# Kernel tuning notes

Hardware: AMD Instinct MI355X
Metric: run time of the kernel (lower is better)

## Reference

```python
import jax, jax.numpy as jnp
import numpy as np

N, H, W, M = 1, 128, 128, 16
HID, STY, CIN, NC, COL = 256, 256, 128, 7, 64


def _lrelu(v):
    return jnp.where(v > 0, v, 0.2 * v)


def _conv(x, w, b=None):
    y = jax.lax.conv_general_dilated(x, w, (1, 1), 'SAME',
                                     dimension_numbers=('NCHW', 'OIHW', 'NCHW'))
    return y if b is None else y + b[None, :, None, None]


def _modlin(f, z, Wt, Wa, ba, Wb, bb):
    # ModLinear, bias=False, mod_bias=True, output_mode=True:
    # y = (f * alpha) @ W^T + beta
    alpha = z @ Wa.T + ba          # [N, in]
    beta = z @ Wb.T + bb           # [N, out]
    return jnp.einsum('nsi,oi->nso', f * alpha[:, None, :], Wt) + beta[:, None, :]


def setup_inputs() -> dict:
    key = jax.random.key(0)
    k = jax.random.split(key, 24)
    s = lambda f: np.float32(1.0 / np.sqrt(f))
    inp = {}
    inp['x'] = jax.random.normal(k[0], (N, H, W, M, CIN), jnp.float32)
    inp['m'] = jax.random.uniform(k[1], (N, H, W, M, NC), jnp.float32)
    inp['z'] = jax.random.normal(k[2], (N, STY), jnp.float32)
    inp['dists'] = jax.random.uniform(k[3], (N, H, W, M), jnp.float32) * 0.05
    # RenderMLP params
    inp['w1'] = jax.random.normal(k[4], (HID, CIN)) * s(CIN)
    inp['b1'] = jnp.zeros((HID,), jnp.float32)
    inp['wma'] = jax.random.normal(k[5], (HID, NC)) * s(NC)
    # 5 stacked ModLinears (fc_2, fc_3, fc_4, fc_5, fc_6)
    inp['ml_w'] = jax.random.normal(k[6], (5, HID, HID)) * s(HID)
    inp['ml_wa'] = jax.random.normal(k[7], (5, HID, STY)) * s(STY)
    inp['ml_ba'] = jnp.ones((5, HID), jnp.float32)
    inp['ml_wb'] = jax.random.normal(k[8], (5, HID, STY)) * s(STY)
    inp['ml_bb'] = jnp.zeros((5, HID), jnp.float32)
    inp['wsig'] = jax.random.normal(k[9], (1, HID)) * s(HID)
    inp['bsig'] = jnp.zeros((1,), jnp.float32)
    inp['wc'] = jax.random.normal(k[10], (COL, HID)) * s(HID)
    inp['bc'] = jnp.zeros((COL,), jnp.float32)
    # RenderCNN params
    inp['wz'] = jax.random.normal(k[11], (4 * HID, STY)) * s(STY)
    inp['bz'] = jnp.zeros((4 * HID,), jnp.float32)
    inp['c1_w'] = jax.random.normal(k[12], (HID, COL, 1, 1)) * s(COL)
    inp['c1_b'] = jnp.zeros((HID,), jnp.float32)
    inp['c2a_w'] = jax.random.normal(k[13], (HID, HID, 3, 3)) * s(HID * 9)
    inp['c2a_b'] = jnp.zeros((HID,), jnp.float32)
    inp['c2b_w'] = jax.random.normal(k[14], (HID, HID, 3, 3)) * s(HID * 9)
    inp['c3a_w'] = jax.random.normal(k[15], (HID, HID, 3, 3)) * s(HID * 9)
    inp['c3a_b'] = jnp.zeros((HID,), jnp.float32)
    inp['c3b_w'] = jax.random.normal(k[16], (HID, HID, 3, 3)) * s(HID * 9)
    inp['c4a_w'] = jax.random.normal(k[17], (HID, HID, 1, 1)) * s(HID)
    inp['c4a_b'] = jnp.zeros((HID,), jnp.float32)
    inp['c4b_w'] = jax.random.normal(k[18], (HID, HID, 1, 1)) * s(HID)
    inp['c4b_b'] = jnp.zeros((HID,), jnp.float32)
    inp['c4_w'] = jax.random.normal(k[19], (3, HID, 1, 1)) * s(HID)
    inp['c4_b'] = jnp.zeros((3,), jnp.float32)
    return inp


def reference(x, m, z, dists, w1, b1, wma, ml_w, ml_wa, ml_ba, ml_wb, ml_bb,
              wsig, bsig, wc, bc, wz, bz, c1_w, c1_b, c2a_w, c2a_b, c2b_w,
              c3a_w, c3a_b, c3b_w, c4a_w, c4a_b, c4b_w, c4b_b, c4_w, c4_b):
    n, h, w_, mm, cin = x.shape
    xf = x.reshape(n, -1, cin)              # [N, S, 128], S = H*W*M
    mf = m.reshape(n, -1, m.shape[-1])      # [N, S, 7]
    # RenderMLP
    f = jnp.einsum('nsi,oi->nso', xf, w1) + b1 + jnp.einsum('nsi,oi->nso', mf, wma)
    f = _lrelu(f)
    for i in range(3):  # fc_2, fc_3, fc_4
        f = _lrelu(_modlin(f, z, ml_w[i], ml_wa[i], ml_ba[i], ml_wb[i], ml_bb[i]))
    sigma = jnp.einsum('nsi,oi->nso', f, wsig) + bsig   # [N, S, 1]
    for i in (3, 4):    # fc_5, fc_6
        f = _lrelu(_modlin(f, z, ml_w[i], ml_wa[i], ml_ba[i], ml_wb[i], ml_bb[i]))
    c = jnp.einsum('nsi,oi->nso', f, wc) + bc           # [N, S, 64]
    # Volumetric alpha compositing along the M ray samples
    sigma = sigma.reshape(n, h, w_, mm)
    c = c.reshape(n, h, w_, mm, -1)
    alpha = 1.0 - jnp.exp(-jax.nn.relu(sigma) * dists)  # [N,H,W,M]
    t = jnp.cumprod(1.0 - alpha + 1e-10, axis=-1)
    t_excl = jnp.concatenate([jnp.ones_like(t[..., :1]), t[..., :-1]], axis=-1)
    wgt = alpha * t_excl
    feat = jnp.einsum('nhwm,nhwmc->nchw', wgt, c)       # [N, 64, H, W]
    # RenderCNN with style modulation
    zc = z @ wz.T + bz
    a0, a1, a2, a3 = jnp.split(zc, 4, axis=-1)
    mod = lambda y, wm, bm: y * (wm[:, :, None, None] + 1.0) + bm[:, :, None, None]
    y = _lrelu(_conv(feat, c1_w, c1_b))
    y = y + _conv(_lrelu(_conv(y, c2a_w, c2a_b)), c2b_w)
    y = _lrelu(mod(y, a0, a1))
    y = y + _conv(_lrelu(_conv(y, c3a_w, c3a_b)), c3b_w)
    y = _lrelu(mod(y, a2, a3))
    y = y + _conv(_lrelu(_conv(y, c4a_w, c4a_b)), c4b_w, c4b_b)
    y = _lrelu(y)
    return _conv(y, c4_w, c4_b)  # [N, 3, H, W]
```

## Files before the change

kernel.cpp:

```cpp
#include <hip/hip_runtime.h>
#include <hip/hip_bf16.h>

#define NPIX 16384
#define S_TOT 262144

typedef __attribute__((ext_vector_type(8))) short bf16x8;
typedef __attribute__((ext_vector_type(4))) float f32x4;

__device__ __forceinline__ float lrelu(float v) { return fmaxf(v, 0.2f * v); }
__device__ __forceinline__ unsigned short f2b(float f) {
  unsigned u = __float_as_uint(f);
  return (unsigned short)((u + 0x7FFFu + ((u >> 16) & 1u)) >> 16);
}
__device__ __forceinline__ unsigned cvtpk(float a, float b) {
  return (unsigned)f2b(a) | ((unsigned)f2b(b) << 16);
}
__device__ __forceinline__ float b2f(short s) {
  return __uint_as_float(((unsigned)(unsigned short)s) << 16);
}
__device__ __forceinline__ float f_lo(int u) { return __uint_as_float((unsigned)u << 16); }
__device__ __forceinline__ float f_hi(int u) { return __uint_as_float((unsigned)u & 0xffff0000u); }

__device__ float g_alpha[5 * 256];
__device__ float g_biasall[1600];
__device__ float g_amod[1024];
__device__ float g_sigma[S_TOT];
__device__ short g_c[S_TOT * 64];
__device__ short g_featb[NPIX * 64];
__device__ short g_y1[NPIX * 256];
__device__ short g_y2[NPIX * 256];
__device__ short g_y3[NPIX * 256];
__device__ short g_t [NPIX * 256];
__device__ short g_wpack[389120];
#define O_C1  0
#define O_C2A 16384
#define O_C2B (16384 + 589824)
#define O_C3A (16384 + 2 * 589824)
#define O_C3B (16384 + 3 * 589824)
#define O_C4A (16384 + 4 * 589824)
#define O_C4B (16384 + 4 * 589824 + 65536)
__device__ short g_wpack2[2506752];

__global__ __launch_bounds__(256) void kparams(const float* __restrict__ z,
    const float* __restrict__ wa, const float* __restrict__ ba,
    const float* __restrict__ wb, const float* __restrict__ bb,
    const float* __restrict__ wz, const float* __restrict__ bz,
    const float* __restrict__ b1, const float* __restrict__ bc) {
  __shared__ float zs[256];
  const int t = threadIdx.x;
  zs[t] = z[t];
  __syncthreads();
  g_biasall[t] = b1[t];
  if (t < 64) g_biasall[1536 + t] = bc[t];
  for (int l = 0; l < 5; ++l) {
    float accA = ba[l * 256 + t];
    float accB = bb[l * 256 + t];
    const float* rowA = wa + (l * 256 + t) * 256;
    const float* rowB = wb + (l * 256 + t) * 256;
    for (int k = 0; k < 256; k += 4) {
      float4 va = *(const float4*)(rowA + k);
      float4 vb = *(const float4*)(rowB + k);
      accA += va.x * zs[k] + va.y * zs[k + 1] + va.z * zs[k + 2] + va.w * zs[k + 3];
      accB += vb.x * zs[k] + vb.y * zs[k + 1] + vb.z * zs[k + 2] + vb.w * zs[k + 3];
    }
    g_alpha[l * 256 + t] = accA;
    g_biasall[256 + l * 256 + t] = accB;
  }
  for (int j = t; j < 1024; j += 256) {
    float acc = bz[j];
    const float* row = wz + j * 256;
    for (int k = 0; k < 256; k += 4) {
      float4 v = *(const float4*)(row + k);
      acc += v.x * zs[k] + v.y * zs[k + 1] + v.z * zs[k + 2] + v.w * zs[k + 3];
    }
    g_amod[j] = acc;
  }
}

__global__ __launch_bounds__(256) void kprep(
    const float* __restrict__ w1, const float* __restrict__ wma,
    const float* __restrict__ mlw, const float* __restrict__ wc,
    const float* __restrict__ wsig) {
  const int idx = blockIdx.x * 256 + threadIdx.x;
  float val;
  if (idx < 40960) {
    int mt = idx / 2560, r2 = idx % 2560;
    int ks = r2 / 512, r = r2 % 512;
    int ln = r >> 3, j = r & 7;
    int oc = mt * 16 + (ln & 15);
    int k = ks * 32 + (ln >> 4) * 8 + j;
    val = (k < 128) ? w1[oc * 128 + k] : ((k < 135) ? wma[oc * 7 + (k - 128)] : 0.f);
  } else if (idx < 368640) {
    int t = idx - 40960;
    int l = t / 65536, t2 = t % 65536;
    int mt = t2 / 4096, r2 = t2 % 4096;
    int ks = r2 / 512, r = r2 % 512;
    int ln = r >> 3, j = r & 7;
    int oc = mt * 16 + (ln & 15);
    int k = ks * 32 + (ln >> 4) * 8 + j;
    val = mlw[l * 65536 + oc * 256 + k] * g_alpha[l * 256 + k];
  } else if (idx < 385024) {
    int t = idx - 368640;
    int mt = t / 4096, r2 = t % 4096;
    int ks = r2 / 512, r = r2 % 512;
    int ln = r >> 3, j = r & 7;
    int oc = mt * 16 + (ln & 15);
    int k = ks * 32 + (ln >> 4) * 8 + j;
    val = wc[oc * 256 + k];
  } else {
    int t = idx - 385024;
    int ks = t / 512, r = t % 512;
    int ln = r >> 3, j = r & 7;
    int row = ln & 15;
    int k = ks * 32 + (ln >> 4) * 8 + j;
    val = (row == 0) ? wsig[k] : 0.f;
  }
  g_wpack[idx] = (short)f2b(val);
}

__global__ __launch_bounds__(256) void kprep_cnn(
    const float* __restrict__ c1w,
    const float* __restrict__ c2aw, const float* __restrict__ c2bw,
    const float* __restrict__ c3aw, const float* __restrict__ c3bw,
    const float* __restrict__ c4aw, const float* __restrict__ c4bw) {
  const int idx = blockIdx.x * 256 + threadIdx.x;
  float val;
  if (idx < 16384) {
    int mt = idx / 1024, r2 = idx % 1024;
    int ks = r2 / 512, r = r2 % 512;
    int ln = r >> 3, j = r & 7;
    int oc = mt * 16 + (ln & 15);
    int k = ks * 32 + (ln >> 4) * 8 + j;
    val = c1w[oc * 64 + k];
  } else if (idx < O_C4A) {
    int t = idx - 16384;
    int cv = t / 589824, t2 = t % 589824;
    const float* w = (cv == 0) ? c2aw : (cv == 1) ? c2bw : (cv == 2) ? c3aw : c3bw;
    int mt = t2 / 36864, r2 = t2 % 36864;
    int ks = r2 / 512, r = r2 % 512;
    int ln = r >> 3, j = r & 7;
    int oc = mt * 16 + (ln & 15);
    int k = ks * 32 + (ln >> 4) * 8 + j;
    int tap = k >> 8, ic = k & 255;
    val = w[oc * 2304 + ic * 9 + tap];
  } else {
    int t = idx - O_C4A;
    const float* w = (t < 65536) ? c4aw : c4bw;
    int t2 = t & 65535;
    int mt = t2 / 4096, r2 = t2 % 4096;
    int ks = r2 / 512, r = r2 % 512;
    int ln = r >> 3, j = r & 7;
    int oc = mt * 16 + (ln & 15);
    int k = ks * 32 + (ln >> 4) * 8 + j;
    val = w[oc * 256 + k];
  }
  g_wpack2[idx] = (short)f2b(val);
}

__device__ __forceinline__ bf16x8 ldsB(const short* buf, int s, int kbyte) {
  const char* p = (const char*)buf + s * 512 + (kbyte ^ ((s & 7) << 4));
  return *(const bf16x8*)p;
}
__device__ __forceinline__ bf16x8 ldA(const short* gA, int frag, int lane) {
  return *(const bf16x8*)(gA + ((size_t)frag << 9) + lane * 8);
}

template<int KS>
__device__ __forceinline__ void layer_gemm(const short* __restrict__ gA,
    const short* __restrict__ inb, short* __restrict__ outb,
    const float* __restrict__ bias, int lane, int wm, int wn) {
  const int lrow = lane & 15;
  const int lkb = (lane >> 4) * 16;
  const int rb = (lane >> 4) * 4;
  f32x4 acc[4][4];
#pragma unroll
  for (int mi = 0; mi < 4; ++mi) {
    const f32x4 bv = *(const f32x4*)(bias + (wm * 4 + mi) * 16 + rb);
#pragma unroll
    for (int ni = 0; ni < 4; ++ni) acc[mi][ni] = bv;
  }
#pragma unroll
  for (int ks = 0; ks < KS; ++ks) {
    bf16x8 A[4], B[4];
#pragma unroll
    for (int mi = 0; mi < 4; ++mi)
      A[mi] = ldA(gA, (wm * 4 + mi) * KS + ks, lane);
#pragma unroll
    for (int ni = 0; ni < 4; ++ni)
      B[ni] = ldsB(inb, wn * 64 + ni * 16 + lrow, ks * 64 + lkb);
#pragma unroll
    for (int mi = 0; mi < 4; ++mi)
#pragma unroll
      for (int ni = 0; ni < 4; ++ni)
        acc[mi][ni] = __builtin_amdgcn_mfma_f32_16x16x32_bf16(A[mi], B[ni], acc[mi][ni], 0, 0, 0);
  }
#pragma unroll
  for (int mi = 0; mi < 4; ++mi) {
    const int oc0 = (wm * 4 + mi) * 16 + rb;
#pragma unroll
    for (int ni = 0; ni < 4; ++ni) {
      const int s = wn * 64 + ni * 16 + lrow;
      f32x4 a = acc[mi][ni];
      char* p = (char*)outb + s * 512 + ((oc0 * 2) ^ ((s & 7) << 4));
      *(int2*)p = make_int2((int)cvtpk(lrelu(a[0]), lrelu(a[1])),
                            (int)cvtpk(lrelu(a[2]), lrelu(a[3])));
    }
  }
}

__global__ __launch_bounds__(512, 1) void kmlp_mfma(
    const float* __restrict__ x, const float* __restrict__ m_in,
    const float* __restrict__ bsig) {
  __shared__ short fbuf[2][32768];
  __shared__ float bias_all[1600];
  const int tid = threadIdx.x;
  const int lane = tid & 63, w = tid >> 6;
  const int wm = w & 3, wn = w >> 2;
  const int s0 = blockIdx.x * 128;

  {
    const float* xp = x + (size_t)s0 * 128;
    const int s = tid >> 2, c = tid & 3;
#pragma unroll
    for (int e = 0; e < 4; ++e) {
      float4 f0 = *(const float4*)(xp + s * 128 + c * 32 + e * 8);
      float4 f1 = *(const float4*)(xp + s * 128 + c * 32 + e * 8 + 4);
      int4 pk;
      pk.x = (int)cvtpk(f0.x, f0.y); pk.y = (int)cvtpk(f0.z, f0.w);
      pk.z = (int)cvtpk(f1.x, f1.y); pk.w = (int)cvtpk(f1.z, f1.w);
      char* p = (char*)fbuf[0] + s * 512 + ((c * 64 + e * 16) ^ ((s & 7) << 4));
      *(int4*)p = pk;
    }
  }
  if (tid < 128) {
    const float* mp = m_in + (size_t)(s0 + tid) * 7;
    float mv[8];
#pragma unroll
    for (int q = 0; q < 7; ++q) mv[q] = mp[q];
    mv[7] = 0.f;
    int4 pk;
    pk.x = (int)cvtpk(mv[0], mv[1]); pk.y = (int)cvtpk(mv[2], mv[3]);
    pk.z = (int)cvtpk(mv[4], mv[5]); pk.w = (int)cvtpk(mv[6], mv[7]);
    char* base = (char*)fbuf[0] + tid * 512;
    const int swz = (tid & 7) << 4;
    *(int4*)(base + (256 ^ swz)) = pk;
    int4 zz = make_int4(0, 0, 0, 0);
    *(int4*)(base + (272 ^ swz)) = zz;
    *(int4*)(base + (288 ^ swz)) = zz;
    *(int4*)(base + (304 ^ swz)) = zz;
  }
  for (int i = tid; i < 1600; i += 512) bias_all[i] = g_biasall[i];
  __syncthreads();

  layer_gemm<5>(g_wpack,                     fbuf[0], fbuf[1], bias_all,        lane, wm, wn);
  __syncthreads();
  layer_gemm<8>(g_wpack + 40960,             fbuf[1], fbuf[0], bias_all + 256,  lane, wm, wn);
  __syncthreads();
  layer_gemm<8>(g_wpack + 40960 + 65536,     fbuf[0], fbuf[1], bias_all + 512,  lane, wm, wn);
  __syncthreads();
  layer_gemm<8>(g_wpack + 40960 + 2 * 65536, fbuf[1], fbuf[0], bias_all + 768,  lane, wm, wn);
  __syncthreads();
  {
    const short* gS = g_wpack + 385024;
    const int lrow = lane & 15, lkb = (lane >> 4) * 16;
    f32x4 sacc = {0.f, 0.f, 0.f, 0.f};
#pragma unroll
    for (int ks = 0; ks < 8; ++ks) {
      bf16x8 A = ldA(gS, ks, lane);
      bf16x8 B = ldsB(fbuf[0], w * 16 + lrow, ks * 64 + lkb);
      sacc = __builtin_amdgcn_mfma_f32_16x16x32_bf16(A, B, sacc, 0, 0, 0);
    }
    if (lane < 16) g_sigma[s0 + w * 16 + lane] = sacc[0] + bsig[0];
  }
  layer_gemm<8>(g_wpack + 40960 + 3 * 65536, fbuf[0], fbuf[1], bias_all + 1024, lane, wm, wn);
  __syncthreads();
  layer_gemm<8>(g_wpack + 40960 + 4 * 65536, fbuf[1], fbuf[0], bias_all + 1280, lane, wm, wn);
  __syncthreads();
  {
    const int lrow = lane & 15, lkb = (lane >> 4) * 16;
    const int rb = (lane >> 4) * 4;
    const int oc0 = wm * 16 + rb;
    const f32x4 bv = *(const f32x4*)(bias_all + 1536 + oc0);
    f32x4 acc[4] = {bv, bv, bv, bv};
    const short* gA = g_wpack + 368640;
#pragma unroll
    for (int ks = 0; ks < 8; ++ks) {
      bf16x8 A = ldA(gA, wm * 8 + ks, lane);
#pragma unroll
      for (int ni = 0; ni < 4; ++ni) {
        bf16x8 B = ldsB(fbuf[0], wn * 64 + ni * 16 + lrow, ks * 64 + lkb);
        acc[ni] = __builtin_amdgcn_mfma_f32_16x16x32_bf16(A, B, acc[ni], 0, 0, 0);
      }
    }
#pragma unroll
    for (int ni = 0; ni < 4; ++ni) {
      const int s = wn * 64 + ni * 16 + lrow;
      *(int2*)(g_c + (size_t)(s0 + s) * 64 + oc0) =
          make_int2((int)cvtpk(acc[ni][0], acc[ni][1]),
                    (int)cvtpk(acc[ni][2], acc[ni][3]));
    }
  }
}

__global__ __launch_bounds__(256) void kcomposite(const float* __restrict__ dists) {
  const int tid = threadIdx.x;
  const int p = blockIdx.x * 4 + (tid >> 6);
  const int ch = tid & 63;
  const int base = p * 16;
  float T = 1.f, acc = 0.f;
  for (int mm = 0; mm < 16; ++mm) {
    float sgm = g_sigma[base + mm];
    float d = dists[base + mm];
    float a = 1.f - expf(-fmaxf(sgm, 0.f) * d);
    acc += a * T * b2f(g_c[(size_t)(base + mm) * 64 + ch]);
    T *= (1.f - a + 1e-10f);
  }
  g_featb[p * 64 + ch] = (short)f2b(acc);
}

template<int IC>
__global__ __launch_bounds__(256, 2) void kgemm1x1(const short* __restrict__ in,
    const short* __restrict__ gA, const float* __restrict__ bias,
    short* __restrict__ out) {
  constexpr int KS = IC / 32;
  constexpr int ROWB = IC * 2;
  __shared__ short binb[32 * IC];
  const int tid = threadIdx.x;
  const int lane = tid & 63, w = tid >> 6;
  const int px0 = blockIdx.x * 32;

  for (int e = tid; e < 32 * IC / 8; e += 256) {
    const int px = e / (IC / 8), lg = e % (IC / 8);
    bf16x8 v = *(const bf16x8*)(in + (size_t)(px0 + px) * IC + lg * 8);
    char* p = (char*)binb + px * ROWB + ((lg * 16) ^ ((px & 7) << 4));
    *(bf16x8*)p = v;
  }
  __syncthreads();

  const int lrow = lane & 15;
  const int lkb = (lane >> 4) * 16;
  const int rb = (lane >> 4) * 4;
  f32x4 acc[4][2];
#pragma unroll
  for (int mi = 0; mi < 4; ++mi) {
    const f32x4 bv = *(const f32x4*)(bias + w * 64 + mi * 16 + rb);
#pragma unroll
    for (int ni = 0; ni < 2; ++ni) acc[mi][ni] = bv;
  }
#pragma unroll
  for (int ks = 0; ks < KS; ++ks) {
    bf16x8 A[4], B[2];
#pragma unroll
    for (int mi = 0; mi < 4; ++mi)
      A[mi] = ldA(gA, (w * 4 + mi) * KS + ks, lane);
#pragma unroll
    for (int ni = 0; ni < 2; ++ni) {
      const int s = ni * 16 + lrow;
      const char* p = (const char*)binb + s * ROWB + ((ks * 64 + lkb) ^ ((s & 7) << 4));
      B[ni] = *(const bf16x8*)p;
    }
#pragma unroll
    for (int mi = 0; mi < 4; ++mi)
#pragma unroll
      for (int ni = 0; ni < 2; ++ni)
        acc[mi][ni] = __builtin_amdgcn_mfma_f32_16x16x32_bf16(A[mi], B[ni], acc[mi][ni], 0, 0, 0);
  }
#pragma unroll
  for (int mi = 0; mi < 4; ++mi) {
    const int oc = w * 64 + mi * 16 + rb;
#pragma unroll
    for (int ni = 0; ni < 2; ++ni) {
      const int gpx = px0 + ni * 16 + lrow;
      f32x4 a = acc[mi][ni];
      *(int2*)(out + (size_t)gpx * 256 + oc) =
          make_int2((int)cvtpk(lrelu(a[0]), lrelu(a[1])),
                    (int)cvtpk(lrelu(a[2]), lrelu(a[3])));
    }
  }
}

__global__ __launch_bounds__(256, 2) void kconv3(const short* __restrict__ in,
    const short* __restrict__ gA, const float* __restrict__ bias,
    const short* __restrict__ res, int domod, const float* __restrict__ modAB,
    short* __restrict__ out) {
  __shared__ short halo[136 * 256];
  const int tid = threadIdx.x;
  const int lane = tid & 63, w = tid >> 6;
  const int oct = blockIdx.x >> 8;
  const int pxt = blockIdx.x & 255;
  const int x0 = (pxt & 3) * 32, y0 = (pxt >> 2) * 2;
  const int oc0 = oct * 128 + w * 32;
  const int lrow = lane & 15;
  const int lkb = (lane >> 4) * 16;
  const int rb = (lane >> 4) * 4;

  for (int e = tid; e < 4352; e += 256) {
    const int row = e >> 5, lg = e & 31;
    const int yy = row / 34, xx = row - yy * 34;
    const int gy = y0 - 1 + yy, gx = x0 - 1 + xx;
    bf16x8 v = {0, 0, 0, 0, 0, 0, 0, 0};
    if (gy >= 0 && gy < 128 && gx >= 0 && gx < 128)
      v = *(const bf16x8*)(in + (size_t)((gy << 7) + gx) * 256 + lg * 8);
    char* p = (char*)halo + row * 512 + ((lg * 16) ^ ((row & 7) << 4));
    *(bf16x8*)p = v;
  }
  __syncthreads();

  const f32x4 zero = {0.f, 0.f, 0.f, 0.f};
  f32x4 acc[2][4];
#pragma unroll
  for (int mi = 0; mi < 2; ++mi) {
    f32x4 bv = zero;
    if (bias) bv = *(const f32x4*)(bias + oc0 + mi * 16 + rb);
#pragma unroll
    for (int ni = 0; ni < 4; ++ni) acc[mi][ni] = bv;
  }

#pragma unroll
  for (int tap = 0; tap < 9; ++tap) {
    const int ky = tap / 3, kx = tap - ky * 3;
#pragma unroll
    for (int s = 0; s < 8; ++s) {
      const int ksg = tap * 8 + s;
      bf16x8 A[2], B[4];
#pragma unroll
      for (int mi = 0; mi < 2; ++mi)
        A[mi] = ldA(gA, (oct * 8 + w * 2 + mi) * 72 + ksg, lane);
#pragma unroll
      for (int ni = 0; ni < 4; ++ni) {
        const int p = ni * 16 + lrow;
        const int row = ((p >> 5) + ky) * 34 + (p & 31) + kx;
        const char* bp = (const char*)halo + row * 512 + ((s * 64 + lkb) ^ ((row & 7) << 4));
        B[ni] = *(const bf16x8*)bp;
      }
#pragma unroll
      for (int mi = 0; mi < 2; ++mi)
#pragma unroll
        for (int ni = 0; ni < 4; ++ni)
          acc[mi][ni] = __builtin_amdgcn_mfma_f32_16x16x32_bf16(A[mi], B[ni], acc[mi][ni], 0, 0, 0);
    }
  }

#pragma unroll
  for (int mi = 0; mi < 2; ++mi) {
    const int oc = oc0 + mi * 16 + rb;
#pragma unroll
    for (int ni = 0; ni < 4; ++ni) {
      const int p = ni * 16 + lrow;
      const int gpx = (y0 + (p >> 5)) * 128 + x0 + (p & 31);
      f32x4 a = acc[mi][ni];
      float v[4] = {a[0], a[1], a[2], a[3]};
      if (res) {
        int2 rv = *(const int2*)(res + (size_t)gpx * 256 + oc);
        v[0] += f_lo(rv.x); v[1] += f_hi(rv.x); v[2] += f_lo(rv.y); v[3] += f_hi(rv.y);
      }
      if (domod) {
#pragma unroll
        for (int r = 0; r < 4; ++r) v[r] = v[r] * (modAB[oc + r] + 1.f) + modAB[256 + oc + r];
      }
      *(int2*)(out + (size_t)gpx * 256 + oc) =
          make_int2((int)cvtpk(lrelu(v[0]), lrelu(v[1])),
                    (int)cvtpk(lrelu(v[2]), lrelu(v[3])));
    }
  }
}

__device__ __forceinline__ void fuse_gemm(const short* __restrict__ inb,
    const short* __restrict__ gA, const float* __restrict__ bias,
    const short* __restrict__ resb, short* __restrict__ outb, int lane, int w) {
  const int lrow = lane & 15;
  const int lkb = (lane >> 4) * 16;
  const int rb = (lane >> 4) * 4;
  f32x4 acc[4][2];
#pragma unroll
  for (int mi = 0; mi < 4; ++mi) {
    const f32x4 bv = *(const f32x4*)(bias + w * 64 + mi * 16 + rb);
#pragma unroll
    for (int ni = 0; ni < 2; ++ni) acc[mi][ni] = bv;
  }
#pragma unroll
  for (int ks = 0; ks < 8; ++ks) {
    bf16x8 A[4], B[2];
#pragma unroll
    for (int mi = 0; mi < 4; ++mi)
      A[mi] = ldA(gA, (w * 4 + mi) * 8 + ks, lane);
#pragma unroll
    for (int ni = 0; ni < 2; ++ni)
      B[ni] = ldsB(inb, ni * 16 + lrow, ks * 64 + lkb);
#pragma unroll
    for (int mi = 0; mi < 4; ++mi)
#pragma unroll
      for (int ni = 0; ni < 2; ++ni)
        acc[mi][ni] = __builtin_amdgcn_mfma_f32_16x16x32_bf16(A[mi], B[ni], acc[mi][ni], 0, 0, 0);
  }
#pragma unroll
  for (int mi = 0; mi < 4; ++mi) {
    const int oc = w * 64 + mi * 16 + rb;
#pragma unroll
    for (int ni = 0; ni < 2; ++ni) {
      const int s = ni * 16 + lrow;
      f32x4 a = acc[mi][ni];
      float v[4] = {a[0], a[1], a[2], a[3]};
      if (resb) {
        const char* rp = (const char*)resb + s * 512 + ((oc * 2) ^ ((s & 7) << 4));
        int2 rv = *(const int2*)rp;
        v[0] += f_lo(rv.x); v[1] += f_hi(rv.x); v[2] += f_lo(rv.y); v[3] += f_hi(rv.y);
      }
      char* p = (char*)outb + s * 512 + ((oc * 2) ^ ((s & 7) << 4));
      *(int2*)p = make_int2((int)cvtpk(lrelu(v[0]), lrelu(v[1])),
                            (int)cvtpk(lrelu(v[2]), lrelu(v[3])));
    }
  }
}

__global__ __launch_bounds__(256, 2) void kc4fuse(const short* __restrict__ y3,
    const short* __restrict__ gA4a, const short* __restrict__ gA4b,
    const float* __restrict__ c4ab, const float* __restrict__ c4bb,
    const float* __restrict__ c4w, const float* __restrict__ c4b,
    float* __restrict__ outp) {
  __shared__ short binb[32 * 256];
  __shared__ short tb[32 * 256];
  __shared__ short yb[32 * 256];
  __shared__ float wl[768];
  __shared__ float sred3[768];
  const int tid = threadIdx.x;
  const int lane = tid & 63, w = tid >> 6;
  const int px0 = blockIdx.x * 32;

  for (int e = tid; e < 1024; e += 256) {
    const int px = e >> 5, lg = e & 31;
    bf16x8 v = *(const bf16x8*)(y3 + (size_t)(px0 + px) * 256 + lg * 8);
    char* p = (char*)binb + px * 512 + ((lg * 16) ^ ((px & 7) << 4));
    *(bf16x8*)p = v;
  }
  for (int i = tid; i < 768; i += 256) wl[i] = c4w[i];
  __syncthreads();

  fuse_gemm(binb, gA4a, c4ab, nullptr, tb, lane, w);
  __syncthreads();
  fuse_gemm(tb, gA4b, c4bb, binb, yb, lane, w);
  __syncthreads();

  {
    const int px = tid >> 3, g = tid & 7;
    float s0 = 0.f, s1 = 0.f, s2 = 0.f;
#pragma unroll
    for (int e = 0; e < 4; ++e) {
      bf16x8 v = ldsB(yb, px, g * 64 + e * 16);
      const int ic0 = g * 32 + e * 8;
#pragma unroll
      for (int j = 0; j < 8; ++j) {
        float f = b2f(v[j]);
        s0 += f * wl[ic0 + j];
        s1 += f * wl[256 + ic0 + j];
        s2 += f * wl[512 + ic0 + j];
      }
    }
    sred3[px * 8 + g] = s0;
    sred3[256 + px * 8 + g] = s1;
    sred3[512 + px * 8 + g] = s2;
  }
  __syncthreads();
  if (tid < 96) {
    const int och = tid >> 5, px = tid & 31;
    const float* sp = sred3 + och * 256 + px * 8;
    float s = sp[0] + sp[1] + sp[2] + sp[3] + sp[4] + sp[5] + sp[6] + sp[7];
    outp[och * NPIX + px0 + px] = s + c4b[och];
  }
}

extern "C" void kernel_launch(void* const* d_in, const int* in_sizes, int n_in,
                              void* d_out, int out_size, void* d_ws, size_t ws_size,
                              hipStream_t stream) {
  (void)in_sizes; (void)n_in; (void)out_size; (void)d_ws; (void)ws_size;
  const float* x    = (const float*)d_in[0];
  const float* m    = (const float*)d_in[1];
  const float* z    = (const float*)d_in[2];
  const float* dists= (const float*)d_in[3];
  const float* w1   = (const float*)d_in[4];
  const float* b1   = (const float*)d_in[5];
  const float* wma  = (const float*)d_in[6];
  const float* mlw  = (const float*)d_in[7];
  const float* mlwa = (const float*)d_in[8];
  const float* mlba = (const float*)d_in[9];
  const float* mlwb = (const float*)d_in[10];
  const float* mlbb = (const float*)d_in[11];
  const float* wsig = (const float*)d_in[12];
  const float* bsig = (const float*)d_in[13];
  const float* wc   = (const float*)d_in[14];
  const float* bc   = (const float*)d_in[15];
  const float* wz   = (const float*)d_in[16];
  const float* bz   = (const float*)d_in[17];
  const float* c1w  = (const float*)d_in[18];
  const float* c1b  = (const float*)d_in[19];
  const float* c2aw = (const float*)d_in[20];
  const float* c2ab = (const float*)d_in[21];
  const float* c2bw = (const float*)d_in[22];
  const float* c3aw = (const float*)d_in[23];
  const float* c3ab = (const float*)d_in[24];
  const float* c3bw = (const float*)d_in[25];
  const float* c4aw = (const float*)d_in[26];
  const float* c4ab = (const float*)d_in[27];
  const float* c4bw = (const float*)d_in[28];
  const float* c4bb = (const float*)d_in[29];
  const float* c4w  = (const float*)d_in[30];
  const float* c4b  = (const float*)d_in[31];
  float* outp = (float*)d_out;

  short *pW2, *pFb, *pY1, *pY2, *pY3, *pT;
  float *pAmod;
  hipGetSymbolAddress((void**)&pW2, HIP_SYMBOL(g_wpack2));
  hipGetSymbolAddress((void**)&pFb, HIP_SYMBOL(g_featb));
  hipGetSymbolAddress((void**)&pY1, HIP_SYMBOL(g_y1));
  hipGetSymbolAddress((void**)&pY2, HIP_SYMBOL(g_y2));
  hipGetSymbolAddress((void**)&pY3, HIP_SYMBOL(g_y3));
  hipGetSymbolAddress((void**)&pT,  HIP_SYMBOL(g_t));
  hipGetSymbolAddress((void**)&pAmod, HIP_SYMBOL(g_amod));

  kparams<<<1, 256, 0, stream>>>(z, mlwa, mlba, mlwb, mlbb, wz, bz, b1, bc);
  kprep<<<1520, 256, 0, stream>>>(w1, wma, mlw, wc, wsig);
  kprep_cnn<<<9792, 256, 0, stream>>>(c1w, c2aw, c2bw, c3aw, c3bw, c4aw, c4bw);
  kmlp_mfma<<<2048, 512, 0, stream>>>(x, m, bsig);
  kcomposite<<<4096, 256, 0, stream>>>(dists);
  kgemm1x1<64> <<<512, 256, 0, stream>>>(pFb, pW2 + O_C1, c1b, pY1);
  kconv3<<<512, 256, 0, stream>>>(pY1, pW2 + O_C2A, c2ab, nullptr, 0, nullptr,    pT);
  kconv3<<<512, 256, 0, stream>>>(pT,  pW2 + O_C2B, nullptr, pY1, 1, pAmod,       pY2);
  kconv3<<<512, 256, 0, stream>>>(pY2, pW2 + O_C3A, c3ab, nullptr, 0, nullptr,    pT);
  kconv3<<<512, 256, 0, stream>>>(pT,  pW2 + O_C3B, nullptr, pY2, 1, pAmod + 512, pY3);
  kc4fuse<<<512, 256, 0, stream>>>(pY3, pW2 + O_C4A, pW2 + O_C4B, c4ab, c4bb, c4w, c4b, outp);
}
```

Measured before the change: 659.6 us.

## Use single in-place LDS feature buffer to allow two MLP blocks per CU

Replaces the ping-pong pair of LDS feature buffers with one buffer updated in place. A barrier between the read phase and the write-back phase makes this safe. This roughly halves LDS use, and together with raising the launch-bounds occupancy hint it lets more blocks share a CU to hide latency. The cost is an extra barrier per layer and a tighter register budget that may cause spills.

```diff
diff --git a/kernel.cpp b/kernel.cpp
--- a/kernel.cpp
+++ b/kernel.cpp
@@ -166,9 +166,8 @@
 }
 
 template<int KS>
-__device__ __forceinline__ void layer_gemm(const short* __restrict__ gA,
-    const short* __restrict__ inb, short* __restrict__ outb,
-    const float* __restrict__ bias, int lane, int wm, int wn) {
+__device__ __forceinline__ void layer_inplace(const short* __restrict__ gA,
+    short* __restrict__ fb, const float* __restrict__ bias, int lane, int wm, int wn) {
   const int lrow = lane & 15;
   const int lkb = (lane >> 4) * 16;
   const int rb = (lane >> 4) * 4;
@@ -187,13 +186,14 @@
       A[mi] = ldA(gA, (wm * 4 + mi) * KS + ks, lane);
 #pragma unroll
     for (int ni = 0; ni < 4; ++ni)
-      B[ni] = ldsB(inb, wn * 64 + ni * 16 + lrow, ks * 64 + lkb);
+      B[ni] = ldsB(fb, wn * 64 + ni * 16 + lrow, ks * 64 + lkb);
 #pragma unroll
     for (int mi = 0; mi < 4; ++mi)
 #pragma unroll
       for (int ni = 0; ni < 4; ++ni)
         acc[mi][ni] = __builtin_amdgcn_mfma_f32_16x16x32_bf16(A[mi], B[ni], acc[mi][ni], 0, 0, 0);
   }
+  __syncthreads();
 #pragma unroll
   for (int mi = 0; mi < 4; ++mi) {
     const int oc0 = (wm * 4 + mi) * 16 + rb;
@@ -201,17 +201,18 @@
     for (int ni = 0; ni < 4; ++ni) {
       const int s = wn * 64 + ni * 16 + lrow;
       f32x4 a = acc[mi][ni];
-      char* p = (char*)outb + s * 512 + ((oc0 * 2) ^ ((s & 7) << 4));
+      char* p = (char*)fb + s * 512 + ((oc0 * 2) ^ ((s & 7) << 4));
       *(int2*)p = make_int2((int)cvtpk(lrelu(a[0]), lrelu(a[1])),
                             (int)cvtpk(lrelu(a[2]), lrelu(a[3])));
     }
   }
-}
-
-__global__ __launch_bounds__(512, 1) void kmlp_mfma(
+  __syncthreads();
+}
+
+__global__ __launch_bounds__(512, 4) void kmlp_mfma(
     const float* __restrict__ x, const float* __restrict__ m_in,
     const float* __restrict__ bsig) {
-  __shared__ short fbuf[2][32768];
+  __shared__ short fbuf[32768];
   __shared__ float bias_all[1600];
   const int tid = threadIdx.x;
   const int lane = tid & 63, w = tid >> 6;
@@ -228,7 +229,7 @@
       int4 pk;
       pk.x = (int)cvtpk(f0.x, f0.y); pk.y = (int)cvtpk(f0.z, f0.w);
       pk.z = (int)cvtpk(f1.x, f1.y); pk.w = (int)cvtpk(f1.z, f1.w);
-      char* p = (char*)fbuf[0] + s * 512 + ((c * 64 + e * 16) ^ ((s & 7) << 4));
+      char* p = (char*)fbuf + s * 512 + ((c * 64 + e * 16) ^ ((s & 7) << 4));
       *(int4*)p = pk;
     }
   }
@@ -241,7 +242,7 @@
     int4 pk;
     pk.x = (int)cvtpk(mv[0], mv[1]); pk.y = (int)cvtpk(mv[2], mv[3]);
     pk.z = (int)cvtpk(mv[4], mv[5]); pk.w = (int)cvtpk(mv[6], mv[7]);
-    char* base = (char*)fbuf[0] + tid * 512;
+    char* base = (char*)fbuf + tid * 512;
     const int swz = (tid & 7) << 4;
     *(int4*)(base + (256 ^ swz)) = pk;
     int4 zz = make_int4(0, 0, 0, 0);
@@ -252,14 +253,16 @@
   for (int i = tid; i < 1600; i += 512) bias_all[i] = g_biasall[i];
   __syncthreads();
 
-  layer_gemm<5>(g_wpack,                     fbuf[0], fbuf[1], bias_all,        lane, wm, wn);
-  __syncthreads();
-  layer_gemm<8>(g_wpack + 40960,             fbuf[1], fbuf[0], bias_all + 256,  lane, wm, wn);
-  __syncthreads();
-  layer_gemm<8>(g_wpack + 40960 + 65536,     fbuf[0], fbuf[1], bias_all + 512,  lane, wm, wn);
-  __syncthreads();
-  layer_gemm<8>(g_wpack + 40960 + 2 * 65536, fbuf[1], fbuf[0], bias_all + 768,  lane, wm, wn);
-  __syncthreads();
+  const short* gF2 = g_wpack + 40960;
+  const short* gF3 = g_wpack + 40960 + 65536;
+  const short* gF4 = g_wpack + 40960 + 2 * 65536;
+  const short* gF5 = g_wpack + 40960 + 3 * 65536;
+  const short* gF6 = g_wpack + 40960 + 4 * 65536;
+
+  layer_inplace<5>(g_wpack, fbuf, bias_all,        lane, wm, wn);
+  layer_inplace<8>(gF2,     fbuf, bias_all + 256,  lane, wm, wn);
+  layer_inplace<8>(gF3,     fbuf, bias_all + 512,  lane, wm, wn);
+  layer_inplace<8>(gF4,     fbuf, bias_all + 768,  lane, wm, wn);
   {
     const short* gS = g_wpack + 385024;
     const int lrow = lane & 15, lkb = (lane >> 4) * 16;
@@ -267,28 +270,26 @@
 #pragma unroll
     for (int ks = 0; ks < 8; ++ks) {
       bf16x8 A = ldA(gS, ks, lane);
-      bf16x8 B = ldsB(fbuf[0], w * 16 + lrow, ks * 64 + lkb);
+      bf16x8 B = ldsB(fbuf, w * 16 + lrow, ks * 64 + lkb);
       sacc = __builtin_amdgcn_mfma_f32_16x16x32_bf16(A, B, sacc, 0, 0, 0);
     }
     if (lane < 16) g_sigma[s0 + w * 16 + lane] = sacc[0] + bsig[0];
   }
-  layer_gemm<8>(g_wpack + 40960 + 3 * 65536, fbuf[0], fbuf[1], bias_all + 1024, lane, wm, wn);
-  __syncthreads();
-  layer_gemm<8>(g_wpack + 40960 + 4 * 65536, fbuf[1], fbuf[0], bias_all + 1280, lane, wm, wn);
-  __syncthreads();
+  layer_inplace<8>(gF5,     fbuf, bias_all + 1024, lane, wm, wn);
+  layer_inplace<8>(gF6,     fbuf, bias_all + 1280, lane, wm, wn);
   {
     const int lrow = lane & 15, lkb = (lane >> 4) * 16;
     const int rb = (lane >> 4) * 4;
     const int oc0 = wm * 16 + rb;
     const f32x4 bv = *(const f32x4*)(bias_all + 1536 + oc0);
     f32x4 acc[4] = {bv, bv, bv, bv};
-    const short* gA = g_wpack + 368640;
+    const short* gC = g_wpack + 368640;
 #pragma unroll
     for (int ks = 0; ks < 8; ++ks) {
-      bf16x8 A = ldA(gA, wm * 8 + ks, lane);
+      bf16x8 A = ldA(gC, wm * 8 + ks, lane);
 #pragma unroll
       for (int ni = 0; ni < 4; ++ni) {
-        bf16x8 B = ldsB(fbuf[0], wn * 64 + ni * 16 + lrow, ks * 64 + lkb);
+        bf16x8 B = ldsB(fbuf, wn * 64 + ni * 16 + lrow, ks * 64 + lkb);
         acc[ni] = __builtin_amdgcn_mfma_f32_16x16x32_bf16(A, B, acc[ni], 0, 0, 0);
       }
     }
```

New measurement: 703.0 us. +6.6%, slower.
